# Optimization experiments

Hardware: AMD Instinct MI355X
Metric: run time of the kernel (lower is better)

## Reference

```python
import jax, jax.numpy as jnp
import numpy as np

V, D, B, NEG = 100000, 128, 4096, 5
D_INNER = int(D * 2.0 * 2 / 3)  # nGPT FF inner dim = 170

def l2norm(t, axis=-1):
    return t / jnp.linalg.norm(t, axis=axis, keepdims=True)

def setup_inputs() -> dict:
    key = jax.random.key(0)
    ks = jax.random.split(key, 8)
    return {
        "input_ids": jax.random.randint(ks[0], (B,), 0, V),
        "target_ids": jax.random.randint(ks[1], (B,), 0, V),
        "neg_ids": jax.random.randint(ks[2], (B, NEG), 0, V),
        "W_in": jax.random.normal(ks[3], (V, D), jnp.float32) * (1.0 / np.sqrt(D)),
        "W_out": jax.random.normal(ks[4], (V, D), jnp.float32) * (1.0 / np.sqrt(D)),
        "W_hidden": jax.random.normal(ks[5], (D_INNER, D), jnp.float32) * 0.02,
        "W_gate": jax.random.normal(ks[6], (D_INNER, D), jnp.float32) * 0.02,
        "W_ff_out": jax.random.normal(ks[7], (D, D_INNER), jnp.float32) * 0.02,
        "hidden_scale": jnp.ones((D_INNER,), jnp.float32),
        "gate_scale": jnp.ones((D_INNER,), jnp.float32),
        "logit_scale": jnp.full((V,), D ** -0.5, dtype=jnp.float32),  # Scale param init = s_logit_scale
    }

def reference(input_ids, target_ids, neg_ids, W_in, W_out, W_hidden, W_gate,
              W_ff_out, hidden_scale, gate_scale, logit_scale):
    # skipgram: gather normalized input embeddings
    emb = l2norm(W_in)[input_ids]                                  # (B, D)
    # nGPT FeedForward: silu-gated, weights l2-normalized on input dim
    h = (emb @ l2norm(W_hidden).T) * hidden_scale                  # (B, D_INNER)
    g = (emb @ l2norm(W_gate).T) * gate_scale * jnp.sqrt(jnp.float32(D))
    x = jax.nn.silu(g) * h
    x = x @ l2norm(W_ff_out, axis=0).T                             # (B, D), to_out norm_dim_in=False
    # logits over full vocab, scaled by Scale(): param * (init/scale)
    scale_eff = logit_scale * (1.0 / (D ** -0.5))                  # (V,)
    logits = (x @ l2norm(W_out).T) * scale_eff                     # (B, V)
    # negative-sampling loss: gather positive + sampled negative logits
    pos = jnp.take_along_axis(logits, target_ids[:, None], axis=1)  # (B, 1)
    neg = jnp.take_along_axis(logits, neg_ids, axis=1)              # (B, NEG)
    positive_loss = jax.nn.log_sigmoid(pos).mean()
    negative_loss = jax.nn.log_sigmoid(-neg).mean()
    return -(positive_loss + negative_loss)
```

## Files before the change

kernel.cpp:

```cpp
#include <hip/hip_runtime.h>
#include <math.h>

#define DD    128
#define DI    170
#define DIP   176
#define ND4   32
#define NI4   43
#define BB    4096
#define NNEG  5
#define ROWS  8
#define NBLK  (BB / ROWS)
#define SQRT_D 11.3137084989847603904f

#define WS_WHT 0
#define WS_WGT (ND4 * DIP * 4)
#define WS_WFT (2 * ND4 * DIP * 4)

__device__ __forceinline__ float wave_bcast_sum(float v) {
#pragma unroll
    for (int m = 1; m < 64; m <<= 1) v += __shfl_xor(v, m, 64);
    return v;
}

__global__ __launch_bounds__(256) void prep_kernel(
    const float* __restrict__ W_hidden,
    const float* __restrict__ W_gate,
    const float* __restrict__ W_ff_out,
    const float* __restrict__ hidden_scale,
    const float* __restrict__ gate_scale,
    float* __restrict__ ws,
    float* __restrict__ out)
{
    if (blockIdx.x == 0 && threadIdx.x == 0) out[0] = 0.0f;
    const int wave = threadIdx.x >> 6;
    const int lane = threadIdx.x & 63;
    const int t = blockIdx.x * 4 + wave;
    float* whT = ws + WS_WHT;
    float* wgT = ws + WS_WGT;
    float* wfT = ws + WS_WFT;

    if (t < DI) {
        const int v = t;
        float a = W_ff_out[(long)(2 * lane)     * DI + v];
        float b = W_ff_out[(long)(2 * lane + 1) * DI + v];
        float cf = wave_bcast_sum(a * a + b * b);
        float2 ph = ((const float2*)(W_hidden + (long)v * DD))[lane];
        float2 pg = ((const float2*)(W_gate   + (long)v * DD))[lane];
        float sh = wave_bcast_sum(ph.x * ph.x + ph.y * ph.y);
        float sg = wave_bcast_sum(pg.x * pg.x + pg.y * pg.y);
        const float whs = rsqrtf(sh) * hidden_scale[v] * rsqrtf(cf);
        const float wgs = rsqrtf(sg) * gate_scale[v] * SQRT_D;
        const int d4   = lane >> 1;
        const int half = lane & 1;
        float2* dh = (float2*)(whT + ((long)d4 * DIP + v) * 4 + half * 2);
        *dh = make_float2(ph.x * whs, ph.y * whs);
        float2* dg = (float2*)(wgT + ((long)d4 * DIP + v) * 4 + half * 2);
        *dg = make_float2(pg.x * wgs, pg.y * wgs);
    } else if (t < DI + NI4) {
        const int i4 = t - DI;
#pragma unroll
        for (int rr = 0; rr < 2; ++rr) {
            const int dd = rr * 64 + lane;
            float4 v4;
            if (i4 < 42) {
                float2 lo = *(const float2*)(W_ff_out + (long)dd * DI + 4 * i4);
                float2 hi = *(const float2*)(W_ff_out + (long)dd * DI + 4 * i4 + 2);
                v4 = make_float4(lo.x, lo.y, hi.x, hi.y);
            } else {
                float2 lo = *(const float2*)(W_ff_out + (long)dd * DI + 168);
                v4 = make_float4(lo.x, lo.y, 0.0f, 0.0f);
            }
            *(float4*)(wfT + ((long)i4 * DD + dd) * 4) = v4;
        }
    } else if (t == DI + NI4 || t == DI + NI4 + 1) {
        float* base = (t == DI + NI4) ? whT : wgT;
        for (int idx = lane; idx < ND4 * 6; idx += 64) {
            const int d4 = idx / 6, c = idx % 6;
            *(float4*)(base + ((long)d4 * DIP + DI + c) * 4) =
                make_float4(0.0f, 0.0f, 0.0f, 0.0f);
        }
    }
}

__global__ __launch_bounds__(256) void main_kernel(
    const int*   __restrict__ input_ids,
    const int*   __restrict__ target_ids,
    const int*   __restrict__ neg_ids,
    const float* __restrict__ W_in,
    const float* __restrict__ W_out,
    const float* __restrict__ logit_scale,
    const float* __restrict__ ws,
    float* __restrict__ out)
{
    __shared__ __align__(16) float s_emb[ROWS][DD];
    __shared__ __align__(16) float s_x[ROWS][DIP];
    __shared__ __align__(16) float s_xout[ROWS][DD];
    __shared__ float s_red[4];

    const int tid  = threadIdx.x;
    const int wave = tid >> 6;
    const int lane = tid & 63;
    const int b0   = blockIdx.x * ROWS;

    const float4* whT4 = (const float4*)(ws + WS_WHT);
    const float4* wgT4 = (const float4*)(ws + WS_WGT);
    const float4* wfT4 = (const float4*)(ws + WS_WFT);

#pragma unroll
    for (int k = 0; k < ROWS / 4; ++k) {
        const int r  = wave + 4 * k;
        const int id = input_ids[b0 + r];
        float2 p = ((const float2*)(W_in + (long)id * DD))[lane];
        float s  = wave_bcast_sum(p.x * p.x + p.y * p.y);
        float inv = rsqrtf(s);
        s_emb[r][2 * lane]     = p.x * inv;
        s_emb[r][2 * lane + 1] = p.y * inv;
    }
    __syncthreads();

    if (tid < DIP) {
        const int i = tid;
        float ah[ROWS], ag[ROWS];
#pragma unroll
        for (int r = 0; r < ROWS; ++r) { ah[r] = 0.0f; ag[r] = 0.0f; }
        for (int d4 = 0; d4 < ND4; ++d4) {
            float4 h4 = whT4[d4 * DIP + i];
            float4 g4 = wgT4[d4 * DIP + i];
#pragma unroll
            for (int r = 0; r < ROWS; ++r) {
                float4 e4 = ((const float4*)s_emb[r])[d4];
                ah[r] += e4.x * h4.x + e4.y * h4.y + e4.z * h4.z + e4.w * h4.w;
                ag[r] += e4.x * g4.x + e4.y * g4.y + e4.z * g4.z + e4.w * g4.w;
            }
        }
#pragma unroll
        for (int r = 0; r < ROWS; ++r) {
            float h = ah[r];
            float g = ag[r];
            float x = (g / (1.0f + __expf(-g))) * h;
            s_x[r][i] = x;
        }
    }
    __syncthreads();

    {
        const int dd = tid & 127;
        const int r0 = tid >> 7;
        float acc[4];
#pragma unroll
        for (int k = 0; k < 4; ++k) acc[k] = 0.0f;
        for (int i4 = 0; i4 < NI4; ++i4) {
            float4 w4 = wfT4[i4 * DD + dd];
#pragma unroll
            for (int k = 0; k < 4; ++k) {
                const int r = r0 + 2 * k;
                float4 x4 = ((const float4*)s_x[r])[i4];
                acc[k] += w4.x * x4.x + w4.y * x4.y + w4.z * x4.z + w4.w * x4.w;
            }
        }
#pragma unroll
        for (int k = 0; k < 4; ++k) s_xout[r0 + 2 * k][dd] = acc[k];
    }
    __syncthreads();

    float wacc = 0.0f;
    for (int t = wave; t < ROWS * (1 + NNEG); t += 4) {
        const int r  = t / (1 + NNEG);
        const int jj = t % (1 + NNEG);
        const int bidx = b0 + r;
        const int id = (jj == 0) ? target_ids[bidx] : neg_ids[bidx * NNEG + jj - 1];
        const float* wrow = W_out + (long)id * DD;
        float w0 = wrow[lane], w1 = wrow[64 + lane];
        float x0 = s_xout[r][lane], x1 = s_xout[r][64 + lane];
        float dot = w0 * x0 + w1 * x1;
        float ss  = w0 * w0 + w1 * w1;
#pragma unroll
        for (int m = 1; m < 64; m <<= 1) {
            dot += __shfl_xor(dot, m, 64);
            ss  += __shfl_xor(ss,  m, 64);
        }
        const float logit = dot * rsqrtf(ss) * logit_scale[id] * SQRT_D;
        const float z  = (jj == 0) ? logit : -logit;
        const float ls = fminf(z, 0.0f) - log1pf(__expf(-fabsf(z)));
        wacc += (jj == 0) ? ls * (1.0f / BB) : ls * (1.0f / (BB * NNEG));
    }
    if (lane == 0) s_red[wave] = wacc;
    __syncthreads();
    if (tid == 0) {
        float tot = s_red[0] + s_red[1] + s_red[2] + s_red[3];
        atomicAdd(out, -tot);
    }
}

extern "C" void kernel_launch(void* const* d_in, const int* in_sizes, int n_in,
                              void* d_out, int out_size, void* d_ws, size_t ws_size,
                              hipStream_t stream) {
    (void)in_sizes; (void)n_in; (void)out_size; (void)ws_size;
    const int*   input_ids    = (const int*)  d_in[0];
    const int*   target_ids   = (const int*)  d_in[1];
    const int*   neg_ids      = (const int*)  d_in[2];
    const float* W_in         = (const float*)d_in[3];
    const float* W_out        = (const float*)d_in[4];
    const float* W_hidden     = (const float*)d_in[5];
    const float* W_gate       = (const float*)d_in[6];
    const float* W_ff_out     = (const float*)d_in[7];
    const float* hidden_scale = (const float*)d_in[8];
    const float* gate_scale   = (const float*)d_in[9];
    const float* logit_scale  = (const float*)d_in[10];
    float* out = (float*)d_out;
    float* ws  = (float*)d_ws;

    prep_kernel<<<54, 256, 0, stream>>>(W_hidden, W_gate, W_ff_out,
                                        hidden_scale, gate_scale, ws, out);
    main_kernel<<<NBLK, 256, 0, stream>>>(input_ids, target_ids, neg_ids,
                                          W_in, W_out, logit_scale, ws, out);
}
```

Before: 166.5 us.

## Double block threads and split hidden/gate projections across thread halves

Main kernel now launches 512 threads per block instead of 256. One half computes the hidden projection and the other the gate projection, and the gate partials are exchanged through a new shared-memory buffer. The output projection and the loss gather are spread over twice as many threads, so each thread carries fewer accumulators. This is meant to raise parallelism and cut per-thread serial work, at the cost of an extra barrier and extra shared memory.

Result: faster. 160.1 us (-3.9%).

```diff
diff --git a/kernel.cpp b/kernel.cpp
--- a/kernel.cpp
+++ b/kernel.cpp
@@ -10,6 +10,7 @@
 #define NNEG  5
 #define ROWS  8
 #define NBLK  (BB / ROWS)
+#define NTHR  512
 #define SQRT_D 11.3137084989847603904f
 
 #define WS_WHT 0
@@ -82,7 +83,7 @@
     }
 }
 
-__global__ __launch_bounds__(256) void main_kernel(
+__global__ __launch_bounds__(NTHR, 4) void main_kernel(
     const int*   __restrict__ input_ids,
     const int*   __restrict__ target_ids,
     const int*   __restrict__ neg_ids,
@@ -95,7 +96,8 @@
     __shared__ __align__(16) float s_emb[ROWS][DD];
     __shared__ __align__(16) float s_x[ROWS][DIP];
     __shared__ __align__(16) float s_xout[ROWS][DD];
-    __shared__ float s_red[4];
+    __shared__ float s_partg[DIP][9];
+    __shared__ float s_red[8];
 
     const int tid  = threadIdx.x;
     const int wave = tid >> 6;
@@ -106,37 +108,46 @@
     const float4* wgT4 = (const float4*)(ws + WS_WGT);
     const float4* wfT4 = (const float4*)(ws + WS_WFT);
 
-#pragma unroll
-    for (int k = 0; k < ROWS / 4; ++k) {
-        const int r  = wave + 4 * k;
-        const int id = input_ids[b0 + r];
+    {
+        const int id = input_ids[b0 + wave];
         float2 p = ((const float2*)(W_in + (long)id * DD))[lane];
         float s  = wave_bcast_sum(p.x * p.x + p.y * p.y);
         float inv = rsqrtf(s);
-        s_emb[r][2 * lane]     = p.x * inv;
-        s_emb[r][2 * lane + 1] = p.y * inv;
-    }
-    __syncthreads();
-
-    if (tid < DIP) {
-        const int i = tid;
-        float ah[ROWS], ag[ROWS];
-#pragma unroll
-        for (int r = 0; r < ROWS; ++r) { ah[r] = 0.0f; ag[r] = 0.0f; }
+        s_emb[wave][2 * lane]     = p.x * inv;
+        s_emb[wave][2 * lane + 1] = p.y * inv;
+    }
+    __syncthreads();
+
+    const bool g0 = (tid < DIP);
+    const bool g1 = (tid >= 256 && tid < 256 + DIP);
+    float a[ROWS];
+#pragma unroll
+    for (int r = 0; r < ROWS; ++r) a[r] = 0.0f;
+    const int i = g0 ? tid : (g1 ? tid - 256 : -1);
+
+    if (i >= 0) {
+        const float4* wT = g0 ? whT4 : wgT4;
+#pragma unroll 4
         for (int d4 = 0; d4 < ND4; ++d4) {
-            float4 h4 = whT4[d4 * DIP + i];
-            float4 g4 = wgT4[d4 * DIP + i];
+            float4 w4 = wT[d4 * DIP + i];
 #pragma unroll
             for (int r = 0; r < ROWS; ++r) {
                 float4 e4 = ((const float4*)s_emb[r])[d4];
-                ah[r] += e4.x * h4.x + e4.y * h4.y + e4.z * h4.z + e4.w * h4.w;
-                ag[r] += e4.x * g4.x + e4.y * g4.y + e4.z * g4.z + e4.w * g4.w;
+                a[r] += e4.x * w4.x + e4.y * w4.y + e4.z * w4.z + e4.w * w4.w;
             }
         }
+    }
+    if (g1) {
+#pragma unroll
+        for (int r = 0; r < ROWS; ++r) s_partg[i][r] = a[r];
+    }
+    __syncthreads();
+
+    if (g0) {
 #pragma unroll
         for (int r = 0; r < ROWS; ++r) {
-            float h = ah[r];
-            float g = ag[r];
+            float h = a[r];
+            float g = s_partg[i][r];
             float x = (g / (1.0f + __expf(-g))) * h;
             s_x[r][i] = x;
         }
@@ -146,25 +157,22 @@
     {
         const int dd = tid & 127;
         const int r0 = tid >> 7;
-        float acc[4];
-#pragma unroll
-        for (int k = 0; k < 4; ++k) acc[k] = 0.0f;
+        float acc0 = 0.0f, acc1 = 0.0f;
+#pragma unroll 4
         for (int i4 = 0; i4 < NI4; ++i4) {
             float4 w4 = wfT4[i4 * DD + dd];
-#pragma unroll
-            for (int k = 0; k < 4; ++k) {
-                const int r = r0 + 2 * k;
-                float4 x4 = ((const float4*)s_x[r])[i4];
-                acc[k] += w4.x * x4.x + w4.y * x4.y + w4.z * x4.z + w4.w * x4.w;
-            }
-        }
-#pragma unroll
-        for (int k = 0; k < 4; ++k) s_xout[r0 + 2 * k][dd] = acc[k];
+            float4 xa = ((const float4*)s_x[r0])[i4];
+            float4 xb = ((const float4*)s_x[r0 + 4])[i4];
+            acc0 += w4.x * xa.x + w4.y * xa.y + w4.z * xa.z + w4.w * xa.w;
+            acc1 += w4.x * xb.x + w4.y * xb.y + w4.z * xb.z + w4.w * xb.w;
+        }
+        s_xout[r0][dd]     = acc0;
+        s_xout[r0 + 4][dd] = acc1;
     }
     __syncthreads();
 
     float wacc = 0.0f;
-    for (int t = wave; t < ROWS * (1 + NNEG); t += 4) {
+    for (int t = wave; t < ROWS * (1 + NNEG); t += 8) {
         const int r  = t / (1 + NNEG);
         const int jj = t % (1 + NNEG);
         const int bidx = b0 + r;
@@ -187,7 +195,8 @@
     if (lane == 0) s_red[wave] = wacc;
     __syncthreads();
     if (tid == 0) {
-        float tot = s_red[0] + s_red[1] + s_red[2] + s_red[3];
+        float tot = s_red[0] + s_red[1] + s_red[2] + s_red[3]
+                  + s_red[4] + s_red[5] + s_red[6] + s_red[7];
         atomicAdd(out, -tot);
     }
 }
@@ -212,6 +221,6 @@
 
     prep_kernel<<<54, 256, 0, stream>>>(W_hidden, W_gate, W_ff_out,
                                         hidden_scale, gate_scale, ws, out);
-    main_kernel<<<NBLK, 256, 0, stream>>>(input_ids, target_ids, neg_ids,
-                                          W_in, W_out, logit_scale, ws, out);
-}
+    main_kernel<<<NBLK, NTHR, 0, stream>>>(input_ids, target_ids, neg_ids,
+                                           W_in, W_out, logit_scale, ws, out);
+}
```

## Restructure main kernel so each wave owns two rows without block barriers

Applied to the files above, without the earlier changes.

Each wave now processes two batch rows end to end: embedding normalization, the hidden/gate projection, the FF output projection and the loss. This removes the __syncthreads barriers between stages and keeps the FF output in registers instead of shared memory. The W_out row loads for all 12 target/negative ids are issued up front with ids broadcast by shuffle, so the gather latency overlaps. The trade-off is that every wave reloads the full FF weight tables from global/L2 for only two rows, cutting weight reuse per load by a factor of four.

New measurement: 161.5 us. 3.0% less time.

```diff
diff --git a/kernel.cpp b/kernel.cpp
--- a/kernel.cpp
+++ b/kernel.cpp
@@ -5,16 +5,21 @@
 #define DI    170
 #define DIP   176
 #define ND4   32
-#define NI4   43
+#define NI4P  44
 #define BB    4096
 #define NNEG  5
-#define ROWS  8
-#define NBLK  (BB / ROWS)
+#define RPW   2
+#define WPB   4
+#define ROWSB (RPW * WPB)
+#define NBLK  (BB / ROWSB)
+#define NTHR  (WPB * 64)
 #define SQRT_D 11.3137084989847603904f
 
 #define WS_WHT 0
 #define WS_WGT (ND4 * DIP * 4)
 #define WS_WFT (2 * ND4 * DIP * 4)
+
+#define DOT4(a, b) ((a).x * (b).x + (a).y * (b).y + (a).z * (b).z + (a).w * (b).w)
 
 __device__ __forceinline__ float wave_bcast_sum(float v) {
 #pragma unroll
@@ -56,7 +61,7 @@
         *dh = make_float2(ph.x * whs, ph.y * whs);
         float2* dg = (float2*)(wgT + ((long)d4 * DIP + v) * 4 + half * 2);
         *dg = make_float2(pg.x * wgs, pg.y * wgs);
-    } else if (t < DI + NI4) {
+    } else if (t < DI + NI4P) {
         const int i4 = t - DI;
 #pragma unroll
         for (int rr = 0; rr < 2; ++rr) {
@@ -66,14 +71,16 @@
                 float2 lo = *(const float2*)(W_ff_out + (long)dd * DI + 4 * i4);
                 float2 hi = *(const float2*)(W_ff_out + (long)dd * DI + 4 * i4 + 2);
                 v4 = make_float4(lo.x, lo.y, hi.x, hi.y);
-            } else {
+            } else if (i4 == 42) {
                 float2 lo = *(const float2*)(W_ff_out + (long)dd * DI + 168);
                 v4 = make_float4(lo.x, lo.y, 0.0f, 0.0f);
+            } else {
+                v4 = make_float4(0.0f, 0.0f, 0.0f, 0.0f);
             }
             *(float4*)(wfT + ((long)i4 * DD + dd) * 4) = v4;
         }
-    } else if (t == DI + NI4 || t == DI + NI4 + 1) {
-        float* base = (t == DI + NI4) ? whT : wgT;
+    } else if (t == DI + NI4P || t == DI + NI4P + 1) {
+        float* base = (t == DI + NI4P) ? whT : wgT;
         for (int idx = lane; idx < ND4 * 6; idx += 64) {
             const int d4 = idx / 6, c = idx % 6;
             *(float4*)(base + ((long)d4 * DIP + DI + c) * 4) =
@@ -82,7 +89,7 @@
     }
 }
 
-__global__ __launch_bounds__(256) void main_kernel(
+__global__ __launch_bounds__(NTHR, 2) void main_kernel(
     const int*   __restrict__ input_ids,
     const int*   __restrict__ target_ids,
     const int*   __restrict__ neg_ids,
@@ -92,94 +99,113 @@
     const float* __restrict__ ws,
     float* __restrict__ out)
 {
-    __shared__ __align__(16) float s_emb[ROWS][DD];
-    __shared__ __align__(16) float s_x[ROWS][DIP];
-    __shared__ __align__(16) float s_xout[ROWS][DD];
-    __shared__ float s_red[4];
+    __shared__ __align__(16) float s_emb[WPB][RPW][DD];
+    __shared__ __align__(16) float s_x[WPB][RPW][DIP];
+    __shared__ float s_red[WPB];
 
     const int tid  = threadIdx.x;
     const int wave = tid >> 6;
     const int lane = tid & 63;
-    const int b0   = blockIdx.x * ROWS;
+    const int rb   = blockIdx.x * ROWSB + wave * RPW;
 
     const float4* whT4 = (const float4*)(ws + WS_WHT);
     const float4* wgT4 = (const float4*)(ws + WS_WGT);
     const float4* wfT4 = (const float4*)(ws + WS_WFT);
 
 #pragma unroll
-    for (int k = 0; k < ROWS / 4; ++k) {
-        const int r  = wave + 4 * k;
-        const int id = input_ids[b0 + r];
+    for (int rr = 0; rr < RPW; ++rr) {
+        const int id = input_ids[rb + rr];
         float2 p = ((const float2*)(W_in + (long)id * DD))[lane];
         float s  = wave_bcast_sum(p.x * p.x + p.y * p.y);
         float inv = rsqrtf(s);
-        s_emb[r][2 * lane]     = p.x * inv;
-        s_emb[r][2 * lane + 1] = p.y * inv;
-    }
-    __syncthreads();
-
-    if (tid < DIP) {
-        const int i = tid;
-        float ah[ROWS], ag[ROWS];
-#pragma unroll
-        for (int r = 0; r < ROWS; ++r) { ah[r] = 0.0f; ag[r] = 0.0f; }
-        for (int d4 = 0; d4 < ND4; ++d4) {
-            float4 h4 = whT4[d4 * DIP + i];
-            float4 g4 = wgT4[d4 * DIP + i];
-#pragma unroll
-            for (int r = 0; r < ROWS; ++r) {
-                float4 e4 = ((const float4*)s_emb[r])[d4];
-                ah[r] += e4.x * h4.x + e4.y * h4.y + e4.z * h4.z + e4.w * h4.w;
-                ag[r] += e4.x * g4.x + e4.y * g4.y + e4.z * g4.z + e4.w * g4.w;
+        s_emb[wave][rr][2 * lane]     = p.x * inv;
+        s_emb[wave][rr][2 * lane + 1] = p.y * inv;
+    }
+
+    float ah[RPW][3], ag[RPW][3];
+#pragma unroll
+    for (int rr = 0; rr < RPW; ++rr)
+#pragma unroll
+        for (int c = 0; c < 3; ++c) { ah[rr][c] = 0.0f; ag[rr][c] = 0.0f; }
+
+#pragma unroll 4
+    for (int d4 = 0; d4 < ND4; ++d4) {
+        float4 e0 = ((const float4*)s_emb[wave][0])[d4];
+        float4 e1 = ((const float4*)s_emb[wave][1])[d4];
+#pragma unroll
+        for (int c = 0; c < 3; ++c) {
+            const int ic = lane + 64 * c;
+            if (ic < DIP) {
+                float4 h4 = whT4[d4 * DIP + ic];
+                float4 g4 = wgT4[d4 * DIP + ic];
+                ah[0][c] += DOT4(e0, h4);
+                ah[1][c] += DOT4(e1, h4);
+                ag[0][c] += DOT4(e0, g4);
+                ag[1][c] += DOT4(e1, g4);
             }
         }
-#pragma unroll
-        for (int r = 0; r < ROWS; ++r) {
-            float h = ah[r];
-            float g = ag[r];
-            float x = (g / (1.0f + __expf(-g))) * h;
-            s_x[r][i] = x;
-        }
-    }
-    __syncthreads();
-
-    {
-        const int dd = tid & 127;
-        const int r0 = tid >> 7;
-        float acc[4];
-#pragma unroll
-        for (int k = 0; k < 4; ++k) acc[k] = 0.0f;
-        for (int i4 = 0; i4 < NI4; ++i4) {
-            float4 w4 = wfT4[i4 * DD + dd];
-#pragma unroll
-            for (int k = 0; k < 4; ++k) {
-                const int r = r0 + 2 * k;
-                float4 x4 = ((const float4*)s_x[r])[i4];
-                acc[k] += w4.x * x4.x + w4.y * x4.y + w4.z * x4.z + w4.w * x4.w;
+    }
+
+#pragma unroll
+    for (int c = 0; c < 3; ++c) {
+        const int ic = lane + 64 * c;
+        if (ic < DIP) {
+#pragma unroll
+            for (int rr = 0; rr < RPW; ++rr) {
+                float h = ah[rr][c];
+                float g = ag[rr][c];
+                s_x[wave][rr][ic] = (g / (1.0f + __expf(-g))) * h;
             }
         }
-#pragma unroll
-        for (int k = 0; k < 4; ++k) s_xout[r0 + 2 * k][dd] = acc[k];
-    }
-    __syncthreads();
-
+    }
+
+    float acc[RPW][2];
+#pragma unroll
+    for (int rr = 0; rr < RPW; ++rr) { acc[rr][0] = 0.0f; acc[rr][1] = 0.0f; }
+#pragma unroll 4
+    for (int i4 = 0; i4 < NI4P; ++i4) {
+        float4 x0 = ((const float4*)s_x[wave][0])[i4];
+        float4 x1 = ((const float4*)s_x[wave][1])[i4];
+        float4 wa = wfT4[i4 * DD + lane];
+        float4 wb = wfT4[i4 * DD + 64 + lane];
+        acc[0][0] += DOT4(x0, wa);
+        acc[0][1] += DOT4(x0, wb);
+        acc[1][0] += DOT4(x1, wa);
+        acc[1][1] += DOT4(x1, wb);
+    }
+
+    int   myid  = 0;
+    float mypsc = 0.0f;
+    if (lane < 2 * (1 + NNEG)) {
+        const int t  = lane;
+        const int rr = t / (1 + NNEG);
+        const int jj = t % (1 + NNEG);
+        const int bidx = rb + rr;
+        myid  = (jj == 0) ? target_ids[bidx] : neg_ids[bidx * NNEG + jj - 1];
+        mypsc = logit_scale[myid];
+    }
+    float w0a[12], w1a[12];
+#pragma unroll
+    for (int t = 0; t < 12; ++t) {
+        const int idt = __shfl(myid, t, 64);
+        const float* wrow = W_out + (long)idt * DD;
+        w0a[t] = wrow[lane];
+        w1a[t] = wrow[64 + lane];
+    }
     float wacc = 0.0f;
-    for (int t = wave; t < ROWS * (1 + NNEG); t += 4) {
-        const int r  = t / (1 + NNEG);
+#pragma unroll
+    for (int t = 0; t < 12; ++t) {
+        const int rr = t / (1 + NNEG);
         const int jj = t % (1 + NNEG);
-        const int bidx = b0 + r;
-        const int id = (jj == 0) ? target_ids[bidx] : neg_ids[bidx * NNEG + jj - 1];
-        const float* wrow = W_out + (long)id * DD;
-        float w0 = wrow[lane], w1 = wrow[64 + lane];
-        float x0 = s_xout[r][lane], x1 = s_xout[r][64 + lane];
-        float dot = w0 * x0 + w1 * x1;
-        float ss  = w0 * w0 + w1 * w1;
+        float dot = w0a[t] * acc[rr][0] + w1a[t] * acc[rr][1];
+        float ss  = w0a[t] * w0a[t] + w1a[t] * w1a[t];
 #pragma unroll
         for (int m = 1; m < 64; m <<= 1) {
             dot += __shfl_xor(dot, m, 64);
             ss  += __shfl_xor(ss,  m, 64);
         }
-        const float logit = dot * rsqrtf(ss) * logit_scale[id] * SQRT_D;
+        const float psc = __shfl(mypsc, t, 64);
+        const float logit = dot * rsqrtf(ss) * psc * SQRT_D;
         const float z  = (jj == 0) ? logit : -logit;
         const float ls = fminf(z, 0.0f) - log1pf(__expf(-fabsf(z)));
         wacc += (jj == 0) ? ls * (1.0f / BB) : ls * (1.0f / (BB * NNEG));
@@ -212,6 +238,6 @@
 
     prep_kernel<<<54, 256, 0, stream>>>(W_hidden, W_gate, W_ff_out,
                                         hidden_scale, gate_scale, ws, out);
-    main_kernel<<<NBLK, 256, 0, stream>>>(input_ids, target_ids, neg_ids,
-                                          W_in, W_out, logit_scale, ws, out);
-}
+    main_kernel<<<NBLK, NTHR, 0, stream>>>(input_ids, target_ids, neg_ids,
+                                           W_in, W_out, logit_scale, ws, out);
+}
```
